# Kernel tuning notes

Measured on AMD Instinct MI355X. Metric: run time of the kernel, lower is better.

Reference implementation:

```python
import jax, jax.numpy as jnp
import numpy as np

INPUT_SIZE, HIDDEN, LEVELS = 64, 256, 2
T, B = 2048, 128


def _lstm_layer(x_seq, h0, c0, W_ih, W_hh, b_ih, b_hh):
    """Run one LSTM layer over the full sequence. x_seq: [T,B,D] -> hs: [T,B,H].
    PyTorch gate order: i, f, g, o."""
    def step(carry, x_t):
        h, c = carry
        z = x_t @ W_ih.T + b_ih + h @ W_hh.T + b_hh  # [B, 4H]
        i, f, g, o = jnp.split(z, 4, axis=-1)
        i = jax.nn.sigmoid(i)
        f = jax.nn.sigmoid(f)
        g = jnp.tanh(g)
        o = jax.nn.sigmoid(o)
        c = f * c + i * g
        h = o * jnp.tanh(c)
        return (h, c), h
    _, hs = jax.lax.scan(step, (h0, c0), x_seq)
    return hs


def setup_inputs() -> dict:
    key = jax.random.key(0)
    ks = jax.random.split(key, 16)
    s = 1.0 / np.sqrt(HIDDEN)
    inp = {
        "x": jax.random.normal(ks[0], (T, B, INPUT_SIZE), dtype=jnp.float32),
        "h0": jax.random.uniform(ks[1], (LEVELS, B, HIDDEN), dtype=jnp.float32),
        "c0": jax.random.uniform(ks[2], (LEVELS, B, HIDDEN), dtype=jnp.float32),
        # layer 0 (input -> hidden)
        "W_ih0": jax.random.uniform(ks[3], (4 * HIDDEN, INPUT_SIZE), jnp.float32, -s, s),
        "W_hh0": jax.random.uniform(ks[4], (4 * HIDDEN, HIDDEN), jnp.float32, -s, s),
        "b_ih0": jax.random.uniform(ks[5], (4 * HIDDEN,), jnp.float32, -s, s),
        "b_hh0": jax.random.uniform(ks[6], (4 * HIDDEN,), jnp.float32, -s, s),
        # layer 1 (hidden -> hidden)
        "W_ih1": jax.random.uniform(ks[7], (4 * HIDDEN, HIDDEN), jnp.float32, -s, s),
        "W_hh1": jax.random.uniform(ks[8], (4 * HIDDEN, HIDDEN), jnp.float32, -s, s),
        "b_ih1": jax.random.uniform(ks[9], (4 * HIDDEN,), jnp.float32, -s, s),
        "b_hh1": jax.random.uniform(ks[10], (4 * HIDDEN,), jnp.float32, -s, s),
        # linear head hidden -> 1
        "W_lin": jax.random.uniform(ks[11], (1, HIDDEN), jnp.float32, -s, s),
        "b_lin": jax.random.uniform(ks[12], (1,), jnp.float32, -s, s),
    }
    return inp


def reference(x, h0, c0, W_ih0, W_hh0, b_ih0, b_hh0, W_ih1, W_hh1, b_ih1, b_hh1, W_lin, b_lin):
    hs0 = _lstm_layer(x, h0[0], c0[0], W_ih0, W_hh0, b_ih0, b_hh0)   # [T,B,H]
    hs1 = _lstm_layer(hs0, h0[1], c0[1], W_ih1, W_hh1, b_ih1, b_hh1)  # [T,B,H]
    out = hs1 @ W_lin.T + b_lin  # [T,B,1]
    return out[..., 0]  # [T,B] (matches torch stack().squeeze())
```

## Files before the change

### kernel.cpp

```cpp
#include <hip/hip_runtime.h>

constexpr int TT   = 2048;
constexpr int NB   = 128;
constexpr int NI   = 64;
constexpr int NH   = 256;
constexpr int NGRP = 128;
constexpr int NWG  = 256;
constexpr int NTHR = 512;
constexpr int R0   = 8;
constexpr int R1   = 16;
constexpr int HLAG = 8;
constexpr int SLOT = (NH / 2) * NB;

__device__ unsigned g_c[64];
__device__ unsigned g_cnt = 0, g_gen = 0;

__device__ __forceinline__ float sigm(float v) { return 1.0f / (1.0f + __expf(-v)); }
__device__ __forceinline__ float tanhfast(float v) {
    float e = __expf(2.0f * v);
    return 1.0f - 2.0f / (e + 1.0f);
}
__device__ __forceinline__ float asfl(unsigned u) { return __uint_as_float(u); }
__device__ __forceinline__ unsigned f2bf(float f) {
    unsigned u = __float_as_uint(f);
    return (u + 0x7fffu + ((u >> 16) & 1u)) >> 16;
}

__device__ __forceinline__ unsigned long long ldq(const unsigned* p) {
    return __hip_atomic_load((const unsigned long long*)p, __ATOMIC_RELAXED,
                             __HIP_MEMORY_SCOPE_AGENT);
}
__device__ __forceinline__ unsigned ldd(const unsigned* p) {
    return __hip_atomic_load(p, __ATOMIC_RELAXED, __HIP_MEMORY_SCOPE_AGENT);
}
__device__ __forceinline__ void std_(unsigned* p, unsigned v) {
    __hip_atomic_store(p, v, __ATOMIC_RELAXED, __HIP_MEMORY_SCOPE_AGENT);
}
__device__ __forceinline__ void bump(unsigned* p) {
    (void)__hip_atomic_fetch_add(p, 1u, __ATOMIC_RELAXED, __HIP_MEMORY_SCOPE_AGENT);
}

__device__ __forceinline__ void poll1(const unsigned* p, unsigned n) {
    for (;;) {
        unsigned v = ldd(p);
        if (__all(v >= n)) return;
        __builtin_amdgcn_s_sleep(1);
    }
}

__device__ __forceinline__ void gridbar(unsigned k, bool last) {
    __syncthreads();
    if (threadIdx.x == 0) {
        __threadfence();
        unsigned a = __hip_atomic_fetch_add(&g_cnt, 1u, __ATOMIC_ACQ_REL,
                                            __HIP_MEMORY_SCOPE_AGENT);
        if (a == k * NWG - 1u) {
            if (last) {
                __hip_atomic_store(&g_cnt, 0u, __ATOMIC_RELAXED, __HIP_MEMORY_SCOPE_AGENT);
                __hip_atomic_store(&g_gen, 0u, __ATOMIC_RELEASE, __HIP_MEMORY_SCOPE_AGENT);
            } else {
                __hip_atomic_store(&g_gen, k, __ATOMIC_RELEASE, __HIP_MEMORY_SCOPE_AGENT);
            }
        } else if (!last) {
            while (__hip_atomic_load(&g_gen, __ATOMIC_RELAXED,
                                     __HIP_MEMORY_SCOPE_AGENT) < k)
                __builtin_amdgcn_s_sleep(1);
        }
        __threadfence();
    }
    __syncthreads();
}

#define STEPQ(Q, HA, HB)                                   \
    acc[0]  += w00.Q * (HA); acc[1]  += w00.Q * (HB);      \
    acc[2]  += w01.Q * (HA); acc[3]  += w01.Q * (HB);      \
    acc[4]  += w02.Q * (HA); acc[5]  += w02.Q * (HB);      \
    acc[6]  += w03.Q * (HA); acc[7]  += w03.Q * (HB);      \
    acc[8]  += w10.Q * (HA); acc[9]  += w10.Q * (HB);      \
    acc[10] += w11.Q * (HA); acc[11] += w11.Q * (HB);      \
    acc[12] += w12.Q * (HA); acc[13] += w12.Q * (HB);      \
    acc[14] += w13.Q * (HA); acc[15] += w13.Q * (HB);

#define LOADW(W, K, kk)                                                        \
    float4 w00 = *(const float4*)((W) + (size_t)(0 * NH + j0    ) * (K) + (kk)); \
    float4 w01 = *(const float4*)((W) + (size_t)(1 * NH + j0    ) * (K) + (kk)); \
    float4 w02 = *(const float4*)((W) + (size_t)(2 * NH + j0    ) * (K) + (kk)); \
    float4 w03 = *(const float4*)((W) + (size_t)(3 * NH + j0    ) * (K) + (kk)); \
    float4 w10 = *(const float4*)((W) + (size_t)(0 * NH + j0 + 1) * (K) + (kk)); \
    float4 w11 = *(const float4*)((W) + (size_t)(1 * NH + j0 + 1) * (K) + (kk)); \
    float4 w12 = *(const float4*)((W) + (size_t)(2 * NH + j0 + 1) * (K) + (kk)); \
    float4 w13 = *(const float4*)((W) + (size_t)(3 * NH + j0 + 1) * (K) + (kk));

__device__ __forceinline__ void partH32(const float* __restrict__ W, int j0,
                                        int kbase,
                                        const unsigned* __restrict__ hd,
                                        int lane, float* acc) {
    const unsigned* hp = hd + (size_t)(kbase >> 1) * NB + (lane << 1);
    #pragma unroll 4
    for (int i = 0; i < 8; ++i) {
        const int kk = kbase + (i << 2);
        LOADW(W, NH, kk)
        unsigned long long q0 = ldq(hp + (size_t)(2 * i) * NB);
        unsigned long long q1 = ldq(hp + (size_t)(2 * i + 1) * NB);
        unsigned d00 = (unsigned)q0, d01 = (unsigned)(q0 >> 32);
        unsigned d10 = (unsigned)q1, d11 = (unsigned)(q1 >> 32);
        STEPQ(x, asfl(d00 << 16),          asfl(d01 << 16))
        STEPQ(y, asfl(d00 & 0xffff0000u),  asfl(d01 & 0xffff0000u))
        STEPQ(z, asfl(d10 << 16),          asfl(d11 << 16))
        STEPQ(w, asfl(d10 & 0xffff0000u),  asfl(d11 & 0xffff0000u))
    }
}

__device__ __forceinline__ void partX8(const float* __restrict__ W, int j0,
                                       int k0, const float* __restrict__ xp,
                                       int lane, float* acc) {
    #pragma unroll
    for (int i4 = 0; i4 < 2; ++i4) {
        const int kk = k0 + (i4 << 2);
        LOADW(W, NI, kk)
        float4 xa = *(const float4*)(xp + (size_t)(lane << 1) * NI + kk);
        float4 xb = *(const float4*)(xp + (size_t)((lane << 1) + 1) * NI + kk);
        STEPQ(x, xa.x, xb.x)
        STEPQ(y, xa.y, xb.y)
        STEPQ(z, xa.z, xb.z)
        STEPQ(w, xa.w, xb.w)
    }
}

__global__ void __launch_bounds__(NTHR, 2) lstm2(
    const float* __restrict__ x,
    const float* __restrict__ h0in, const float* __restrict__ c0in,
    const float* __restrict__ Wih0, const float* __restrict__ Whh0,
    const float* __restrict__ bih0, const float* __restrict__ bhh0,
    const float* __restrict__ Wih1, const float* __restrict__ Whh1,
    const float* __restrict__ bih1, const float* __restrict__ bhh1,
    const float* __restrict__ Wlin, const float* __restrict__ blin,
    float* __restrict__ out,
    unsigned* __restrict__ h0d, unsigned* __restrict__ h1d)
{
    __shared__ __align__(16) float4 zp4[16 * NB];
    __shared__ float red[4];
    __shared__ unsigned go_w;

    const int tid  = threadIdx.x;
    const int gid  = blockIdx.x;
    const bool is1 = gid >= NGRP;
    const int g    = is1 ? gid - NGRP : gid;
    const int j0   = g * 2;
    const int lane = tid & 63;
    const int wv   = __builtin_amdgcn_readfirstlane(tid >> 6);

    unsigned* ownc = is1 ? &g_c[32] : &g_c[0];

    float4 bsA = make_float4(0, 0, 0, 0), bsB = bsA;
    float cA = 0.f, cB = 0.f;
    if (tid < 128) {
        const float* bi = is1 ? bih1 : bih0;
        const float* bh = is1 ? bhh1 : bhh0;
        bsA.x = bi[0 * NH + j0] + bh[0 * NH + j0];
        bsA.y = bi[1 * NH + j0] + bh[1 * NH + j0];
        bsA.z = bi[2 * NH + j0] + bh[2 * NH + j0];
        bsA.w = bi[3 * NH + j0] + bh[3 * NH + j0];
        bsB.x = bi[0 * NH + j0 + 1] + bh[0 * NH + j0 + 1];
        bsB.y = bi[1 * NH + j0 + 1] + bh[1 * NH + j0 + 1];
        bsB.z = bi[2 * NH + j0 + 1] + bh[2 * NH + j0 + 1];
        bsB.w = bi[3 * NH + j0 + 1] + bh[3 * NH + j0 + 1];
        const float* cbase = c0in + (is1 ? 1 : 0) * NB * NH + (size_t)tid * NH + j0;
        cA = cbase[0]; cB = cbase[1];
        const float* hbase = h0in + (is1 ? 1 : 0) * NB * NH + (size_t)tid * NH + j0;
        unsigned d = (f2bf(hbase[1]) << 16) | f2bf(hbase[0]);
        unsigned* hT = is1 ? h1d : h0d;
        const int islot = is1 ? (R1 - 1) : (R0 - 1);
        std_(hT + (size_t)islot * SLOT + (size_t)g * NB + tid, d);
    }
    if (tid == 0) go_w = 0;
    const float blv = blin[0];
    asm volatile("s_waitcnt vmcnt(0)" ::: "memory");
    __syncthreads();
    if (tid == 0) bump(ownc);

    if (!is1) {
        for (int s = 0; s < TT + HLAG; ++s) {
            const unsigned gA = 2u * (unsigned)s + 1u;
            const unsigned gB = gA + 1u;
            if (wv == 0) {
                if (s >= R0) poll1(&g_c[32], 128u * (unsigned)(s - R0 + 2));
                if (lane == 0)
                    __hip_atomic_store(&go_w, gA, __ATOMIC_RELAXED,
                                       __HIP_MEMORY_SCOPE_WORKGROUP);
            } else {
                while (__hip_atomic_load(&go_w, __ATOMIC_RELAXED,
                                         __HIP_MEMORY_SCOPE_WORKGROUP) < gA) {}
            }

            float acc[16] = {0,0,0,0,0,0,0,0,0,0,0,0,0,0,0,0};
            if (s < TT)
                partX8(Wih0, j0, wv * 8, x + (size_t)s * NB * NI, lane, acc);

            if (s >= HLAG && tid >= 256) {
                const int u = s - HLAG;
                const int k = tid - 256;
                unsigned d = ldd(h1d + (size_t)(u & (R1 - 1)) * SLOT
                                 + (size_t)(k >> 1) * NB + g);
                float hv = (k & 1) ? asfl(d & 0xffff0000u) : asfl(d << 16);
                float p = Wlin[k] * hv;
                #pragma unroll
                for (int off = 32; off; off >>= 1) p += __shfl_down(p, off);
                if (lane == 0) red[wv - 4] = p;
            }

            if (s < TT) {
                if (wv == 0) {
                    poll1(&g_c[0], 128u * (unsigned)(s + 1));
                    if (lane == 0)
                        __hip_atomic_store(&go_w, gB, __ATOMIC_RELAXED,
                                           __HIP_MEMORY_SCOPE_WORKGROUP);
                } else {
                    while (__hip_atomic_load(&go_w, __ATOMIC_RELAXED,
                                             __HIP_MEMORY_SCOPE_WORKGROUP) < gB) {}
                }
                partH32(Whh0, j0, wv * 32,
                        h0d + (size_t)((s + R0 - 1) & (R0 - 1)) * SLOT, lane, acc);
                const int base0 = ((wv << 1) + 0) * NB + (lane << 1);
                const int base1 = ((wv << 1) + 1) * NB + (lane << 1);
                zp4[base0]     = make_float4(acc[0],  acc[2],  acc[4],  acc[6]);
                zp4[base0 + 1] = make_float4(acc[1],  acc[3],  acc[5],  acc[7]);
                zp4[base1]     = make_float4(acc[8],  acc[10], acc[12], acc[14]);
                zp4[base1 + 1] = make_float4(acc[9],  acc[11], acc[13], acc[15]);
            }
            __syncthreads();

            if (s < TT && tid < 128) {
                float4 zA = bsA, zB = bsB;
                #pragma unroll
                for (int q = 0; q < 8; ++q) {
                    float4 a = zp4[(q * 2 + 0) * NB + tid];
                    float4 b = zp4[(q * 2 + 1) * NB + tid];
                    zA.x += a.x; zA.y += a.y; zA.z += a.z; zA.w += a.w;
                    zB.x += b.x; zB.y += b.y; zB.z += b.z; zB.w += b.w;
                }
                float iA = sigm(zA.x), fA = sigm(zA.y), gA2 = tanhfast(zA.z), oA = sigm(zA.w);
                cA = fA * cA + iA * gA2;
                float hA = oA * tanhfast(cA);
                float iB = sigm(zB.x), fB = sigm(zB.y), gB2 = tanhfast(zB.z), oB = sigm(zB.w);
                cB = fB * cB + iB * gB2;
                float hB = oB * tanhfast(cB);
                unsigned d = (f2bf(hB) << 16) | f2bf(hA);
                std_(h0d + (size_t)(s & (R0 - 1)) * SLOT + (size_t)g * NB + tid, d);
            }
            if (s >= HLAG && tid == 256)
                out[(size_t)(s - HLAG) * NB + g] = red[0] + red[1] + red[2] + red[3] + blv;

            asm volatile("s_waitcnt vmcnt(0)" ::: "memory");
            __syncthreads();
            if (s < TT && tid == 0) bump(&g_c[0]);
        }
    } else {
        for (int t = 0; t < TT; ++t) {
            const unsigned gA = 2u * (unsigned)t + 1u;
            const unsigned gB = gA + 1u;
            if (wv == 0) {
                poll1(&g_c[0], 128u * (unsigned)(t + 2));
                if (lane == 0)
                    __hip_atomic_store(&go_w, gA, __ATOMIC_RELAXED,
                                       __HIP_MEMORY_SCOPE_WORKGROUP);
            } else {
                while (__hip_atomic_load(&go_w, __ATOMIC_RELAXED,
                                         __HIP_MEMORY_SCOPE_WORKGROUP) < gA) {}
            }

            float acc[16] = {0,0,0,0,0,0,0,0,0,0,0,0,0,0,0,0};
            partH32(Wih1, j0, wv * 32,
                    h0d + (size_t)(t & (R0 - 1)) * SLOT, lane, acc);

            if (wv == 0) {
                poll1(&g_c[32], 128u * (unsigned)(t + 1));
                if (lane == 0)
                    __hip_atomic_store(&go_w, gB, __ATOMIC_RELAXED,
                                       __HIP_MEMORY_SCOPE_WORKGROUP);
            } else {
                while (__hip_atomic_load(&go_w, __ATOMIC_RELAXED,
                                         __HIP_MEMORY_SCOPE_WORKGROUP) < gB) {}
            }
            partH32(Whh1, j0, wv * 32,
                    h1d + (size_t)((t + R1 - 1) & (R1 - 1)) * SLOT, lane, acc);
            const int base0 = ((wv << 1) + 0) * NB + (lane << 1);
            const int base1 = ((wv << 1) + 1) * NB + (lane << 1);
            zp4[base0]     = make_float4(acc[0],  acc[2],  acc[4],  acc[6]);
            zp4[base0 + 1] = make_float4(acc[1],  acc[3],  acc[5],  acc[7]);
            zp4[base1]     = make_float4(acc[8],  acc[10], acc[12], acc[14]);
            zp4[base1 + 1] = make_float4(acc[9],  acc[11], acc[13], acc[15]);
            __syncthreads();

            if (tid < 128) {
                float4 zA = bsA, zB = bsB;
                #pragma unroll
                for (int q = 0; q < 8; ++q) {
                    float4 a = zp4[(q * 2 + 0) * NB + tid];
                    float4 b = zp4[(q * 2 + 1) * NB + tid];
                    zA.x += a.x; zA.y += a.y; zA.z += a.z; zA.w += a.w;
                    zB.x += b.x; zB.y += b.y; zB.z += b.z; zB.w += b.w;
                }
                float iA = sigm(zA.x), fA = sigm(zA.y), gA2 = tanhfast(zA.z), oA = sigm(zA.w);
                cA = fA * cA + iA * gA2;
                float hA = oA * tanhfast(cA);
                float iB = sigm(zB.x), fB = sigm(zB.y), gB2 = tanhfast(zB.z), oB = sigm(zB.w);
                cB = fB * cB + iB * gB2;
                float hB = oB * tanhfast(cB);
                unsigned d = (f2bf(hB) << 16) | f2bf(hA);
                std_(h1d + (size_t)(t & (R1 - 1)) * SLOT + (size_t)g * NB + tid, d);
            }
            asm volatile("s_waitcnt vmcnt(0)" ::: "memory");
            __syncthreads();
            if (tid == 0) bump(&g_c[32]);
        }
    }

    gridbar(1, false);
    if (gid == 0 && tid == 0) {
        __hip_atomic_store(&g_c[0],  0u, __ATOMIC_RELAXED, __HIP_MEMORY_SCOPE_AGENT);
        __hip_atomic_store(&g_c[32], 0u, __ATOMIC_RELAXED, __HIP_MEMORY_SCOPE_AGENT);
    }
    gridbar(2, true);
}

extern "C" void kernel_launch(void* const* d_in, const int* in_sizes, int n_in,
                              void* d_out, int out_size, void* d_ws, size_t ws_size,
                              hipStream_t stream)
{
    const float* x    = (const float*)d_in[0];
    const float* h0in = (const float*)d_in[1];
    const float* c0in = (const float*)d_in[2];
    const float* Wih0 = (const float*)d_in[3];
    const float* Whh0 = (const float*)d_in[4];
    const float* bih0 = (const float*)d_in[5];
    const float* bhh0 = (const float*)d_in[6];
    const float* Wih1 = (const float*)d_in[7];
    const float* Whh1 = (const float*)d_in[8];
    const float* bih1 = (const float*)d_in[9];
    const float* bhh1 = (const float*)d_in[10];
    const float* Wlin = (const float*)d_in[11];
    const float* blin = (const float*)d_in[12];
    float* out = (float*)d_out;

    unsigned* h0d = (unsigned*)d_ws;
    unsigned* h1d = h0d + (size_t)R0 * SLOT;

    void* args[] = { &x, &h0in, &c0in, &Wih0, &Whh0, &bih0, &bhh0,
                     &Wih1, &Whh1, &bih1, &bhh1, &Wlin, &blin,
                     &out, &h0d, &h1d };
    hipLaunchCooperativeKernel((void*)lstm2, dim3(NWG), dim3(NTHR), args, 0, stream);
}
```

Baseline: 20.34 ms.

## Spread gate combine across all waves and drop end-of-step barrier with double-buffered LDS

The gate-combine work moves from the first 128 threads to 16 lanes in each of the 8 waves. Each wave then bumps the global step counter on its own, and poll targets rise from 128 to 1024 per step. With this, the second __syncthreads per step is removed, and the LDS partial-sum and reduction buffers are double-buffered by step parity to avoid races. The aim is to take a block-wide barrier off the serial recurrence critical path. The cost is eight times more atomic traffic on the global counters, with less lane utilisation in the combine phase.

```diff
diff --git a/kernel.cpp b/kernel.cpp
--- a/kernel.cpp
+++ b/kernel.cpp
@@ -138,8 +138,8 @@
     float* __restrict__ out,
     unsigned* __restrict__ h0d, unsigned* __restrict__ h1d)
 {
-    __shared__ __align__(16) float4 zp4[16 * NB];
-    __shared__ float red[4];
+    __shared__ __align__(16) float4 zp4[2][16 * NB];
+    __shared__ float red[2][4];
     __shared__ unsigned go_w;
 
     const int tid  = threadIdx.x;
@@ -149,12 +149,14 @@
     const int j0   = g * 2;
     const int lane = tid & 63;
     const int wv   = __builtin_amdgcn_readfirstlane(tid >> 6);
+    const bool cmb = (lane < 16);
+    const int bcol = wv * 16 + lane;
 
     unsigned* ownc = is1 ? &g_c[32] : &g_c[0];
 
     float4 bsA = make_float4(0, 0, 0, 0), bsB = bsA;
     float cA = 0.f, cB = 0.f;
-    if (tid < 128) {
+    if (cmb) {
         const float* bi = is1 ? bih1 : bih0;
         const float* bh = is1 ? bhh1 : bhh0;
         bsA.x = bi[0 * NH + j0] + bh[0 * NH + j0];
@@ -165,26 +167,26 @@
         bsB.y = bi[1 * NH + j0 + 1] + bh[1 * NH + j0 + 1];
         bsB.z = bi[2 * NH + j0 + 1] + bh[2 * NH + j0 + 1];
         bsB.w = bi[3 * NH + j0 + 1] + bh[3 * NH + j0 + 1];
-        const float* cbase = c0in + (is1 ? 1 : 0) * NB * NH + (size_t)tid * NH + j0;
+        const float* cbase = c0in + (is1 ? 1 : 0) * NB * NH + (size_t)bcol * NH + j0;
         cA = cbase[0]; cB = cbase[1];
-        const float* hbase = h0in + (is1 ? 1 : 0) * NB * NH + (size_t)tid * NH + j0;
+        const float* hbase = h0in + (is1 ? 1 : 0) * NB * NH + (size_t)bcol * NH + j0;
         unsigned d = (f2bf(hbase[1]) << 16) | f2bf(hbase[0]);
         unsigned* hT = is1 ? h1d : h0d;
         const int islot = is1 ? (R1 - 1) : (R0 - 1);
-        std_(hT + (size_t)islot * SLOT + (size_t)g * NB + tid, d);
+        std_(hT + (size_t)islot * SLOT + (size_t)g * NB + bcol, d);
     }
     if (tid == 0) go_w = 0;
     const float blv = blin[0];
     asm volatile("s_waitcnt vmcnt(0)" ::: "memory");
     __syncthreads();
-    if (tid == 0) bump(ownc);
+    if (lane == 0) bump(ownc);
 
     if (!is1) {
         for (int s = 0; s < TT + HLAG; ++s) {
             const unsigned gA = 2u * (unsigned)s + 1u;
             const unsigned gB = gA + 1u;
             if (wv == 0) {
-                if (s >= R0) poll1(&g_c[32], 128u * (unsigned)(s - R0 + 2));
+                if (s >= R0) poll1(&g_c[32], 1024u * (unsigned)(s - R0 + 2));
                 if (lane == 0)
                     __hip_atomic_store(&go_w, gA, __ATOMIC_RELAXED,
                                        __HIP_MEMORY_SCOPE_WORKGROUP);
@@ -206,12 +208,12 @@
                 float p = Wlin[k] * hv;
                 #pragma unroll
                 for (int off = 32; off; off >>= 1) p += __shfl_down(p, off);
-                if (lane == 0) red[wv - 4] = p;
+                if (lane == 0) red[s & 1][wv - 4] = p;
             }
 
             if (s < TT) {
                 if (wv == 0) {
-                    poll1(&g_c[0], 128u * (unsigned)(s + 1));
+                    poll1(&g_c[0], 1024u * (unsigned)(s + 1));
                     if (lane == 0)
                         __hip_atomic_store(&go_w, gB, __ATOMIC_RELAXED,
                                            __HIP_MEMORY_SCOPE_WORKGROUP);
@@ -221,21 +223,23 @@
                 }
                 partH32(Whh0, j0, wv * 32,
                         h0d + (size_t)((s + R0 - 1) & (R0 - 1)) * SLOT, lane, acc);
+                float4* zw = zp4[s & 1];
                 const int base0 = ((wv << 1) + 0) * NB + (lane << 1);
                 const int base1 = ((wv << 1) + 1) * NB + (lane << 1);
-                zp4[base0]     = make_float4(acc[0],  acc[2],  acc[4],  acc[6]);
-                zp4[base0 + 1] = make_float4(acc[1],  acc[3],  acc[5],  acc[7]);
-                zp4[base1]     = make_float4(acc[8],  acc[10], acc[12], acc[14]);
-                zp4[base1 + 1] = make_float4(acc[9],  acc[11], acc[13], acc[15]);
+                zw[base0]     = make_float4(acc[0],  acc[2],  acc[4],  acc[6]);
+                zw[base0 + 1] = make_float4(acc[1],  acc[3],  acc[5],  acc[7]);
+                zw[base1]     = make_float4(acc[8],  acc[10], acc[12], acc[14]);
+                zw[base1 + 1] = make_float4(acc[9],  acc[11], acc[13], acc[15]);
             }
             __syncthreads();
 
-            if (s < TT && tid < 128) {
+            if (s < TT && cmb) {
+                const float4* zr = zp4[s & 1];
                 float4 zA = bsA, zB = bsB;
                 #pragma unroll
                 for (int q = 0; q < 8; ++q) {
-                    float4 a = zp4[(q * 2 + 0) * NB + tid];
-                    float4 b = zp4[(q * 2 + 1) * NB + tid];
+                    float4 a = zr[(q * 2 + 0) * NB + bcol];
+                    float4 b = zr[(q * 2 + 1) * NB + bcol];
                     zA.x += a.x; zA.y += a.y; zA.z += a.z; zA.w += a.w;
                     zB.x += b.x; zB.y += b.y; zB.z += b.z; zB.w += b.w;
                 }
@@ -246,21 +250,22 @@
                 cB = fB * cB + iB * gB2;
                 float hB = oB * tanhfast(cB);
                 unsigned d = (f2bf(hB) << 16) | f2bf(hA);
-                std_(h0d + (size_t)(s & (R0 - 1)) * SLOT + (size_t)g * NB + tid, d);
-            }
-            if (s >= HLAG && tid == 256)
-                out[(size_t)(s - HLAG) * NB + g] = red[0] + red[1] + red[2] + red[3] + blv;
+                std_(h0d + (size_t)(s & (R0 - 1)) * SLOT + (size_t)g * NB + bcol, d);
+            }
+            if (s >= HLAG && tid == 256) {
+                float* r = red[s & 1];
+                out[(size_t)(s - HLAG) * NB + g] = r[0] + r[1] + r[2] + r[3] + blv;
+            }
 
             asm volatile("s_waitcnt vmcnt(0)" ::: "memory");
-            __syncthreads();
-            if (s < TT && tid == 0) bump(&g_c[0]);
+            if (s < TT && lane == 0) bump(&g_c[0]);
         }
     } else {
         for (int t = 0; t < TT; ++t) {
             const unsigned gA = 2u * (unsigned)t + 1u;
             const unsigned gB = gA + 1u;
             if (wv == 0) {
-                poll1(&g_c[0], 128u * (unsigned)(t + 2));
+                poll1(&g_c[0], 1024u * (unsigned)(t + 2));
                 if (lane == 0)
                     __hip_atomic_store(&go_w, gA, __ATOMIC_RELAXED,
                                        __HIP_MEMORY_SCOPE_WORKGROUP);
@@ -274,7 +279,7 @@
                     h0d + (size_t)(t & (R0 - 1)) * SLOT, lane, acc);
 
             if (wv == 0) {
-                poll1(&g_c[32], 128u * (unsigned)(t + 1));
+                poll1(&g_c[32], 1024u * (unsigned)(t + 1));
                 if (lane == 0)
                     __hip_atomic_store(&go_w, gB, __ATOMIC_RELAXED,
                                        __HIP_MEMORY_SCOPE_WORKGROUP);
@@ -284,20 +289,22 @@
             }
             partH32(Whh1, j0, wv * 32,
                     h1d + (size_t)((t + R1 - 1) & (R1 - 1)) * SLOT, lane, acc);
+            float4* zw = zp4[t & 1];
             const int base0 = ((wv << 1) + 0) * NB + (lane << 1);
             const int base1 = ((wv << 1) + 1) * NB + (lane << 1);
-            zp4[base0]     = make_float4(acc[0],  acc[2],  acc[4],  acc[6]);
-            zp4[base0 + 1] = make_float4(acc[1],  acc[3],  acc[5],  acc[7]);
-            zp4[base1]     = make_float4(acc[8],  acc[10], acc[12], acc[14]);
-            zp4[base1 + 1] = make_float4(acc[9],  acc[11], acc[13], acc[15]);
+            zw[base0]     = make_float4(acc[0],  acc[2],  acc[4],  acc[6]);
+            zw[base0 + 1] = make_float4(acc[1],  acc[3],  acc[5],  acc[7]);
+            zw[base1]     = make_float4(acc[8],  acc[10], acc[12], acc[14]);
+            zw[base1 + 1] = make_float4(acc[9],  acc[11], acc[13], acc[15]);
             __syncthreads();
 
-            if (tid < 128) {
+            if (cmb) {
+                const float4* zr = zp4[t & 1];
                 float4 zA = bsA, zB = bsB;
                 #pragma unroll
                 for (int q = 0; q < 8; ++q) {
-                    float4 a = zp4[(q * 2 + 0) * NB + tid];
-                    float4 b = zp4[(q * 2 + 1) * NB + tid];
+                    float4 a = zr[(q * 2 + 0) * NB + bcol];
+                    float4 b = zr[(q * 2 + 1) * NB + bcol];
                     zA.x += a.x; zA.y += a.y; zA.z += a.z; zA.w += a.w;
                     zB.x += b.x; zB.y += b.y; zB.z += b.z; zB.w += b.w;
                 }
@@ -308,11 +315,10 @@
                 cB = fB * cB + iB * gB2;
                 float hB = oB * tanhfast(cB);
                 unsigned d = (f2bf(hB) << 16) | f2bf(hA);
-                std_(h1d + (size_t)(t & (R1 - 1)) * SLOT + (size_t)g * NB + tid, d);
+                std_(h1d + (size_t)(t & (R1 - 1)) * SLOT + (size_t)g * NB + bcol, d);
             }
             asm volatile("s_waitcnt vmcnt(0)" ::: "memory");
-            __syncthreads();
-            if (tid == 0) bump(&g_c[32]);
+            if (lane == 0) bump(&g_c[32]);
         }
     }
 
```

Result: slower. 59.89 ms (+194.4%).
